# Performance work log

Hardware: AMD Instinct MI355X
Metric: run time of the kernel (lower is better)

Reference implementation:

```python
import jax, jax.numpy as jnp
import numpy as np

BETA = 0.9      # leak factor
THR = 1.0       # snntorch Leaky default threshold
ALPHA = 2.0     # snntorch ATan surrogate default alpha

@jax.custom_vjp
def spike(x):
    # Heaviside fire; surrogate gradient (ATan) on backward, as in snntorch.
    return (x > 0).astype(x.dtype)

def _spike_fwd(x):
    return spike(x), x

def _spike_bwd(x, g):
    return (g * (ALPHA / 2.0) / (1.0 + (jnp.pi / 2.0 * ALPHA * x) ** 2),)

spike.defvjp(_spike_fwd, _spike_bwd)

def setup_inputs() -> dict:
    key = jax.random.key(0)
    ks = jax.random.split(key, 7)
    B, T, I, H, O = 512, 200, 784, 128, 10
    def lin(k, fan_out, fan_in):
        bound = 1.0 / np.sqrt(fan_in)
        return jax.random.uniform(k, (fan_out, fan_in), jnp.float32, -bound, bound)
    return {
        "x": jax.random.normal(ks[0], (B, T, I), jnp.float32),
        "W1": lin(ks[1], H, I), "b1": jax.random.uniform(ks[2], (H,), jnp.float32, -1/np.sqrt(I), 1/np.sqrt(I)),
        "W2": lin(ks[3], H, H), "b2": jax.random.uniform(ks[4], (H,), jnp.float32, -1/np.sqrt(H), 1/np.sqrt(H)),
        "W3": lin(ks[5], O, H), "b3": jax.random.uniform(ks[6], (O,), jnp.float32, -1/np.sqrt(H), 1/np.sqrt(H)),
    }

def reference(x, W1, b1, W2, b2, W3, b3):
    B = x.shape[0]
    H, O = W2.shape[0], W3.shape[0]
    xt = jnp.swapaxes(x, 0, 1)  # [T, B, I] for scan over time

    def lif(cur, mem, spk_prev):
        # snntorch Leaky (reset-by-subtraction, reset computed from previous mem):
        # mem_new = beta*mem + cur - spk_prev*thr ; spk = heaviside(mem_new - thr)
        mem = BETA * mem + cur - spk_prev * THR
        return spike(mem - THR), mem

    def step(carry, inp):
        m1, s1, m2, s2, m3, s3 = carry
        s1, m1 = lif(inp @ W1.T + b1, m1, s1)
        s2, m2 = lif(s1 @ W2.T + b2, m2, s2)
        s3, m3 = lif(s2 @ W3.T + b3, m3, s3)
        return (m1, s1, m2, s2, m3, s3), s3

    z = lambda d: jnp.zeros((B, d), x.dtype)
    init = (z(H), z(H), z(H), z(H), z(O), z(O))
    _, spk_rec = jax.lax.scan(step, init, xt)
    return spk_rec  # [T, B, num_outputs], matches torch.stack(spk_rec, dim=0)
```

## Files before the change

kernel.cpp:

```cpp
#include <hip/hip_runtime.h>

namespace {
constexpr int kB = 512;
constexpr int kT = 200;
constexpr int kI = 784;
constexpr int kH = 128;
constexpr int kO = 10;
constexpr int kM = kB * kT;
constexpr float kBeta = 0.9f;
constexpr float kThr = 1.0f;
}

template <int K>
__global__ __launch_bounds__(256, 2) void gemm_nt128(
    const float* __restrict__ A, const float* __restrict__ B,
    const float* __restrict__ bias, float* __restrict__ C) {
  constexpr int BM = 128, BK = 16;
  __shared__ float As[BK][BM + 4];
  __shared__ float Bs[BK][BM + 4];
  const int tid = threadIdx.x;
  const int tx = tid & 15;
  const int ty = tid >> 4;
  const int row0 = blockIdx.x * BM;

  float acc[8][8];
#pragma unroll
  for (int i = 0; i < 8; ++i)
#pragma unroll
    for (int j = 0; j < 8; ++j) acc[i][j] = 0.0f;

  for (int k0 = 0; k0 < K; k0 += BK) {
    __syncthreads();
#pragma unroll
    for (int l = 0; l < 2; ++l) {
      const int fi = tid + l * 256;
      const int row = fi >> 2;
      const int c4 = (fi & 3) * 4;
      const float4 va = *reinterpret_cast<const float4*>(
          &A[(size_t)(row0 + row) * K + k0 + c4]);
      As[c4 + 0][row] = va.x;
      As[c4 + 1][row] = va.y;
      As[c4 + 2][row] = va.z;
      As[c4 + 3][row] = va.w;
      const float4 vb = *reinterpret_cast<const float4*>(
          &B[(size_t)row * K + k0 + c4]);
      Bs[c4 + 0][row] = vb.x;
      Bs[c4 + 1][row] = vb.y;
      Bs[c4 + 2][row] = vb.z;
      Bs[c4 + 3][row] = vb.w;
    }
    __syncthreads();
#pragma unroll
    for (int kk = 0; kk < BK; ++kk) {
      float a[8], b[8];
      *reinterpret_cast<float4*>(&a[0]) =
          *reinterpret_cast<const float4*>(&As[kk][ty * 4]);
      *reinterpret_cast<float4*>(&a[4]) =
          *reinterpret_cast<const float4*>(&As[kk][64 + ty * 4]);
      *reinterpret_cast<float4*>(&b[0]) =
          *reinterpret_cast<const float4*>(&Bs[kk][tx * 4]);
      *reinterpret_cast<float4*>(&b[4]) =
          *reinterpret_cast<const float4*>(&Bs[kk][64 + tx * 4]);
#pragma unroll
      for (int i = 0; i < 8; ++i)
#pragma unroll
        for (int j = 0; j < 8; ++j) acc[i][j] = fmaf(a[i], b[j], acc[i][j]);
    }
  }

#pragma unroll
  for (int i = 0; i < 8; ++i) {
    const int m = (i < 4) ? (ty * 4 + i) : (64 + ty * 4 + (i - 4));
    const size_t r = (size_t)(row0 + m);
#pragma unroll
    for (int jh = 0; jh < 2; ++jh) {
      const int n = jh * 64 + tx * 4;
      float4 v;
      v.x = acc[i][jh * 4 + 0] + bias[n + 0];
      v.y = acc[i][jh * 4 + 1] + bias[n + 1];
      v.z = acc[i][jh * 4 + 2] + bias[n + 2];
      v.w = acc[i][jh * 4 + 3] + bias[n + 3];
      *reinterpret_cast<float4*>(&C[r * 128 + n]) = v;
    }
  }
}

__global__ __launch_bounds__(256) void lif_scan(float* __restrict__ buf) {
  const int g = blockIdx.x * 256 + threadIdx.x;
  const int b = g >> 7;
  const int h = g & 127;
  const size_t base = (size_t)b * kT * 128 + h;
  float m = 0.0f, s = 0.0f;
#pragma unroll 4
  for (int t = 0; t < kT; ++t) {
    const float cur = buf[base + (size_t)t * 128];
    m = __fsub_rn(__fadd_rn(__fmul_rn(kBeta, m), cur), s);
    s = (m > kThr) ? 1.0f : 0.0f;
    buf[base + (size_t)t * 128] = s;
  }
}

__global__ __launch_bounds__(320) void gemm3_n10(
    const float* __restrict__ A, const float* __restrict__ W3,
    const float* __restrict__ b3, float* __restrict__ C) {
  __shared__ float Ss[64][132];
  __shared__ float Ws[10][132];
  __shared__ float bs[10];
  const int tid = threadIdx.x;
  const size_t row0 = (size_t)blockIdx.x * 64;

  {
    const int r = tid >> 5;
    const int c4 = (tid & 31) * 4;
    const float4 v = *reinterpret_cast<const float4*>(&W3[r * 128 + c4]);
    Ws[r][c4 + 0] = v.x;
    Ws[r][c4 + 1] = v.y;
    Ws[r][c4 + 2] = v.z;
    Ws[r][c4 + 3] = v.w;
    if (tid < 10) bs[tid] = b3[tid];
  }
  for (int fi = tid; fi < 2048; fi += 320) {
    const int r = fi >> 5;
    const int c4 = (fi & 31) * 4;
    const float4 v =
        *reinterpret_cast<const float4*>(&A[(row0 + r) * 128 + c4]);
    Ss[r][c4 + 0] = v.x;
    Ss[r][c4 + 1] = v.y;
    Ss[r][c4 + 2] = v.z;
    Ss[r][c4 + 3] = v.w;
  }
  __syncthreads();

#pragma unroll
  for (int l = 0; l < 2; ++l) {
    const int idx = tid + l * 320;
    const int r = idx / 10;
    const int o = idx - r * 10;
    float acc = bs[o];
#pragma unroll
    for (int k = 0; k < 128; k += 4) {
      const float4 a = *reinterpret_cast<const float4*>(&Ss[r][k]);
      const float4 w = *reinterpret_cast<const float4*>(&Ws[o][k]);
      acc = fmaf(a.x, w.x, acc);
      acc = fmaf(a.y, w.y, acc);
      acc = fmaf(a.z, w.z, acc);
      acc = fmaf(a.w, w.w, acc);
    }
    C[(row0 + r) * 10 + o] = acc;
  }
}

__global__ __launch_bounds__(256) void lif_scan_out(
    const float* __restrict__ cur3, float* __restrict__ out) {
  const int g = blockIdx.x * 256 + threadIdx.x;
  if (g >= kB * kO) return;
  const int b = g / kO;
  const int o = g - b * kO;
  float m = 0.0f, s = 0.0f;
#pragma unroll 4
  for (int t = 0; t < kT; ++t) {
    const float c = cur3[((size_t)b * kT + t) * kO + o];
    m = __fsub_rn(__fadd_rn(__fmul_rn(kBeta, m), c), s);
    s = (m > kThr) ? 1.0f : 0.0f;
    out[(size_t)t * (kB * kO) + g] = s;
  }
}

extern "C" void kernel_launch(void* const* d_in, const int* in_sizes, int n_in,
                              void* d_out, int out_size, void* d_ws,
                              size_t ws_size, hipStream_t stream) {
  (void)in_sizes;
  (void)n_in;
  (void)out_size;
  (void)ws_size;
  const float* x = (const float*)d_in[0];
  const float* W1 = (const float*)d_in[1];
  const float* b1 = (const float*)d_in[2];
  const float* W2 = (const float*)d_in[3];
  const float* b2 = (const float*)d_in[4];
  const float* W3 = (const float*)d_in[5];
  const float* b3 = (const float*)d_in[6];
  float* out = (float*)d_out;

  float* buf0 = (float*)d_ws;
  float* buf1 = buf0 + (size_t)kM * kH;
  float* cur3 = buf0;

  gemm_nt128<kI><<<kM / 128, 256, 0, stream>>>(x, W1, b1, buf0);
  lif_scan<<<(kB * kH) / 256, 256, 0, stream>>>(buf0);
  gemm_nt128<kH><<<kM / 128, 256, 0, stream>>>(buf0, W2, b2, buf1);
  lif_scan<<<(kB * kH) / 256, 256, 0, stream>>>(buf1);
  gemm3_n10<<<kM / 64, 320, 0, stream>>>(buf1, W3, b3, cur3);
  lif_scan_out<<<(kB * kO + 255) / 256, 256, 0, stream>>>(cur3, out);
}
```

Before: 424.1 us.

## Split-K the first GEMM into two halves and fold partial sums into a vectorized LIF scan

The large 784-wide input GEMM is split along K into two partial-sum blocks per tile, doubling grid size to improve occupancy and load balance. The two partials and bias are summed inside the layer-1 LIF scan, which now processes four neurons per thread with float4 loads/stores; the layer-2 scan is vectorized similarly. The cost is an extra 52 MB partial buffer written and read, and the scans have 4x fewer threads, which reduces parallelism for latency-bound serial loops.

After: 418.0 us. No clear change (-1.4%).

```diff
diff --git a/kernel.cpp b/kernel.cpp
--- a/kernel.cpp
+++ b/kernel.cpp
@@ -9,19 +9,41 @@
 constexpr int kM = kB * kT;
 constexpr float kBeta = 0.9f;
 constexpr float kThr = 1.0f;
-}
-
-template <int K>
-__global__ __launch_bounds__(256, 2) void gemm_nt128(
+constexpr int kSplitK0 = 400;
+}
+
+template <int KSTRIDE, int SPLIT>
+__global__ __launch_bounds__(256, 2) void gemm_part(
     const float* __restrict__ A, const float* __restrict__ B,
-    const float* __restrict__ bias, float* __restrict__ C) {
+    const float* __restrict__ bias, float* __restrict__ C, size_t coff) {
   constexpr int BM = 128, BK = 16;
   __shared__ float As[BK][BM + 4];
   __shared__ float Bs[BK][BM + 4];
   const int tid = threadIdx.x;
   const int tx = tid & 15;
   const int ty = tid >> 4;
-  const int row0 = blockIdx.x * BM;
+  int tile, kbeg, nsteps;
+  if (SPLIT) {
+    tile = blockIdx.x >> 1;
+    const int half = blockIdx.x & 1;
+    kbeg = half ? kSplitK0 : 0;
+    nsteps = half ? (KSTRIDE - kSplitK0) / BK : kSplitK0 / BK;
+    if (half) C += coff;
+  } else {
+    tile = blockIdx.x;
+    kbeg = 0;
+    nsteps = KSTRIDE / BK;
+  }
+  const int row0 = tile * BM;
+
+  const int srow0 = tid >> 2;
+  const int srow1 = srow0 + 64;
+  const int sc4 = (tid & 3) * 4;
+
+  const float* aptr0 = A + (size_t)(row0 + srow0) * KSTRIDE + kbeg + sc4;
+  const float* aptr1 = A + (size_t)(row0 + srow1) * KSTRIDE + kbeg + sc4;
+  const float* bptr0 = B + (size_t)srow0 * KSTRIDE + kbeg + sc4;
+  const float* bptr1 = B + (size_t)srow1 * KSTRIDE + kbeg + sc4;
 
   float acc[8][8];
 #pragma unroll
@@ -29,25 +51,22 @@
 #pragma unroll
     for (int j = 0; j < 8; ++j) acc[i][j] = 0.0f;
 
-  for (int k0 = 0; k0 < K; k0 += BK) {
+  for (int s = 0; s < nsteps; ++s) {
+    const int k0 = s * BK;
     __syncthreads();
-#pragma unroll
-    for (int l = 0; l < 2; ++l) {
-      const int fi = tid + l * 256;
-      const int row = fi >> 2;
-      const int c4 = (fi & 3) * 4;
-      const float4 va = *reinterpret_cast<const float4*>(
-          &A[(size_t)(row0 + row) * K + k0 + c4]);
-      As[c4 + 0][row] = va.x;
-      As[c4 + 1][row] = va.y;
-      As[c4 + 2][row] = va.z;
-      As[c4 + 3][row] = va.w;
-      const float4 vb = *reinterpret_cast<const float4*>(
-          &B[(size_t)row * K + k0 + c4]);
-      Bs[c4 + 0][row] = vb.x;
-      Bs[c4 + 1][row] = vb.y;
-      Bs[c4 + 2][row] = vb.z;
-      Bs[c4 + 3][row] = vb.w;
+    {
+      const float4 va0 = *reinterpret_cast<const float4*>(aptr0 + k0);
+      const float4 va1 = *reinterpret_cast<const float4*>(aptr1 + k0);
+      const float4 vb0 = *reinterpret_cast<const float4*>(bptr0 + k0);
+      const float4 vb1 = *reinterpret_cast<const float4*>(bptr1 + k0);
+      As[sc4 + 0][srow0] = va0.x; As[sc4 + 1][srow0] = va0.y;
+      As[sc4 + 2][srow0] = va0.z; As[sc4 + 3][srow0] = va0.w;
+      As[sc4 + 0][srow1] = va1.x; As[sc4 + 1][srow1] = va1.y;
+      As[sc4 + 2][srow1] = va1.z; As[sc4 + 3][srow1] = va1.w;
+      Bs[sc4 + 0][srow0] = vb0.x; Bs[sc4 + 1][srow0] = vb0.y;
+      Bs[sc4 + 2][srow0] = vb0.z; Bs[sc4 + 3][srow0] = vb0.w;
+      Bs[sc4 + 0][srow1] = vb1.x; Bs[sc4 + 1][srow1] = vb1.y;
+      Bs[sc4 + 2][srow1] = vb1.z; Bs[sc4 + 3][srow1] = vb1.w;
     }
     __syncthreads();
 #pragma unroll
@@ -76,27 +95,67 @@
     for (int jh = 0; jh < 2; ++jh) {
       const int n = jh * 64 + tx * 4;
       float4 v;
-      v.x = acc[i][jh * 4 + 0] + bias[n + 0];
-      v.y = acc[i][jh * 4 + 1] + bias[n + 1];
-      v.z = acc[i][jh * 4 + 2] + bias[n + 2];
-      v.w = acc[i][jh * 4 + 3] + bias[n + 3];
+      v.x = acc[i][jh * 4 + 0];
+      v.y = acc[i][jh * 4 + 1];
+      v.z = acc[i][jh * 4 + 2];
+      v.w = acc[i][jh * 4 + 3];
+      if (bias != nullptr) {
+        v.x += bias[n + 0];
+        v.y += bias[n + 1];
+        v.z += bias[n + 2];
+        v.w += bias[n + 3];
+      }
       *reinterpret_cast<float4*>(&C[r * 128 + n]) = v;
     }
   }
 }
 
-__global__ __launch_bounds__(256) void lif_scan(float* __restrict__ buf) {
+__global__ __launch_bounds__(256) void lif_scan13(
+    float* __restrict__ P0, const float* __restrict__ P1,
+    const float* __restrict__ b1) {
   const int g = blockIdx.x * 256 + threadIdx.x;
-  const int b = g >> 7;
-  const int h = g & 127;
-  const size_t base = (size_t)b * kT * 128 + h;
-  float m = 0.0f, s = 0.0f;
-#pragma unroll 4
+  const int b = g >> 5;
+  const int h4 = (g & 31) * 4;
+  const size_t base = (size_t)b * kT * 128 + h4;
+  const float4 bb = *reinterpret_cast<const float4*>(&b1[h4]);
+  float4 m = {0.f, 0.f, 0.f, 0.f}, s = {0.f, 0.f, 0.f, 0.f};
   for (int t = 0; t < kT; ++t) {
-    const float cur = buf[base + (size_t)t * 128];
-    m = __fsub_rn(__fadd_rn(__fmul_rn(kBeta, m), cur), s);
-    s = (m > kThr) ? 1.0f : 0.0f;
-    buf[base + (size_t)t * 128] = s;
+    const size_t idx = base + (size_t)t * 128;
+    const float4 c0 = *reinterpret_cast<const float4*>(&P0[idx]);
+    const float4 c1 = *reinterpret_cast<const float4*>(&P1[idx]);
+    float4 sp;
+#define LIF1(c)                                                        \
+  {                                                                    \
+    const float cur = __fadd_rn(__fadd_rn(c0.c, c1.c), bb.c);          \
+    m.c = __fsub_rn(__fadd_rn(__fmul_rn(kBeta, m.c), cur), s.c);       \
+    sp.c = (m.c > kThr) ? 1.0f : 0.0f;                                 \
+  }
+    LIF1(x) LIF1(y) LIF1(z) LIF1(w)
+#undef LIF1
+    s = sp;
+    *reinterpret_cast<float4*>(&P0[idx]) = sp;
+  }
+}
+
+__global__ __launch_bounds__(256) void lif_scan2(float* __restrict__ buf) {
+  const int g = blockIdx.x * 256 + threadIdx.x;
+  const int b = g >> 5;
+  const int h4 = (g & 31) * 4;
+  const size_t base = (size_t)b * kT * 128 + h4;
+  float4 m = {0.f, 0.f, 0.f, 0.f}, s = {0.f, 0.f, 0.f, 0.f};
+  for (int t = 0; t < kT; ++t) {
+    const size_t idx = base + (size_t)t * 128;
+    const float4 c0 = *reinterpret_cast<const float4*>(&buf[idx]);
+    float4 sp;
+#define LIF1(c)                                                        \
+  {                                                                    \
+    m.c = __fsub_rn(__fadd_rn(__fmul_rn(kBeta, m.c), c0.c), s.c);      \
+    sp.c = (m.c > kThr) ? 1.0f : 0.0f;                                 \
+  }
+    LIF1(x) LIF1(y) LIF1(z) LIF1(w)
+#undef LIF1
+    s = sp;
+    *reinterpret_cast<float4*>(&buf[idx]) = sp;
   }
 }
 
@@ -182,14 +241,15 @@
   const float* b3 = (const float*)d_in[6];
   float* out = (float*)d_out;
 
-  float* buf0 = (float*)d_ws;
-  float* buf1 = buf0 + (size_t)kM * kH;
-  float* cur3 = buf0;
-
-  gemm_nt128<kI><<<kM / 128, 256, 0, stream>>>(x, W1, b1, buf0);
-  lif_scan<<<(kB * kH) / 256, 256, 0, stream>>>(buf0);
-  gemm_nt128<kH><<<kM / 128, 256, 0, stream>>>(buf0, W2, b2, buf1);
-  lif_scan<<<(kB * kH) / 256, 256, 0, stream>>>(buf1);
-  gemm3_n10<<<kM / 64, 320, 0, stream>>>(buf1, W3, b3, cur3);
-  lif_scan_out<<<(kB * kO + 255) / 256, 256, 0, stream>>>(cur3, out);
-}
+  const size_t bufElems = (size_t)kM * kH;
+  float* P0 = (float*)d_ws;
+  float* P1 = P0 + bufElems;
+
+  gemm_part<kI, 1><<<2 * (kM / 128), 256, 0, stream>>>(
+      x, W1, nullptr, P0, bufElems);
+  lif_scan13<<<(kB * kH / 4) / 256, 256, 0, stream>>>(P0, P1, b1);
+  gemm_part<kH, 0><<<kM / 128, 256, 0, stream>>>(P0, W2, b2, P1, 0);
+  lif_scan2<<<(kB * kH / 4) / 256, 256, 0, stream>>>(P1);
+  gemm3_n10<<<kM / 64, 320, 0, stream>>>(P1, W3, b3, P0);
+  lif_scan_out<<<(kB * kO + 255) / 256, 256, 0, stream>>>(P0, out);
+}
```
